# Kernel optimization log

Measured on AMD Instinct MI355X. Metric: run time of the kernel, lower is better.

Reference implementation:

```python
import jax, jax.numpy as jnp
import numpy as np

N_EXPERTS = 8
TOP_K = 2

def setup_inputs() -> dict:
    key = jax.random.key(0)
    ks = jax.random.split(key, 7)
    d, h, e = 1024, 4096, N_EXPERTS
    x = jax.random.normal(ks[0], (4, 2048, d), dtype=jnp.float32)
    gate_w = jax.random.normal(ks[1], (d, e), dtype=jnp.float32) * (1.0 / np.sqrt(d))
    gate_b = jnp.zeros((e,), dtype=jnp.float32)
    w1 = jax.random.normal(ks[2], (e, d, h), dtype=jnp.float32) * (1.0 / np.sqrt(d))
    b1 = jnp.zeros((e, h), dtype=jnp.float32)
    w2 = jax.random.normal(ks[3], (e, h, d), dtype=jnp.float32) * (1.0 / np.sqrt(h))
    b2 = jnp.zeros((e, d), dtype=jnp.float32)
    return {"x": x, "gate_w": gate_w, "gate_b": gate_b,
            "w1": w1, "b1": b1, "w2": w2, "b2": b2}

def reference(x, gate_w, gate_b, w1, b1, w2, b2):
    B, T, C = x.shape
    xf = x.reshape(-1, C)                                  # [N, C]
    gate_logits = xf @ gate_w + gate_b                     # [N, E]
    top_vals, top_idx = jax.lax.top_k(gate_logits, TOP_K)  # [N, K]
    top_w = jax.nn.softmax(top_vals, axis=-1)              # softmax over selected logits
    out = jnp.zeros_like(xf)
    for i in range(N_EXPERTS):
        # per-token combine weight for expert i (0 if not in top-k)
        wi = jnp.sum(jnp.where(top_idx == i, top_w, 0.0), axis=-1)  # [N]
        h = jax.nn.gelu(xf @ w1[i] + b1[i], approximate=False)      # [N, 4C]
        y = h @ w2[i] + b2[i]                                       # [N, C]
        out = out + wi[:, None] * y
    return out.reshape(B, T, C)
```

## Files before the change

kernel.cpp:

```cpp
#include <hip/hip_runtime.h>
#include <math.h>


#define NTOK 8192
#define CDIM 1024
#define HDIM 4096
#define NEXP 8
#define MAXT2 71
#define MAXROWS2 (MAXT2 * 256)
#define G1BLK (MAXT2 * 16)
#define TRBLK 512

typedef unsigned short u16;
typedef __attribute__((ext_vector_type(8))) _Float16 half8;
typedef __attribute__((ext_vector_type(4))) float f32x4;

__device__ __forceinline__ u16 f2h(float f) {
    union { _Float16 h; u16 u; } cv; cv.h = (_Float16)f; return cv.u;
}
__device__ __forceinline__ float h2f(u16 u) {
    union { u16 u; _Float16 h; } cv; cv.u = u; return (float)cv.h;
}
__device__ __forceinline__ void gll16(const u16* g, u16* l) {
    __builtin_amdgcn_global_load_lds((__attribute__((address_space(1))) void*)(g),
                                     (__attribute__((address_space(3))) void*)(l),
                                     16, 0, 0);
}
__device__ __forceinline__ float gelu_f(float v) {
    float u = 0.70710678118654752f * v;
    float au = fabsf(u);
    float t = __builtin_amdgcn_rcpf(1.0f + 0.3275911f * au);
    float p = t * (0.254829592f + t * (-0.284496736f + t * (1.421413741f +
              t * (-1.453152027f + t * 1.061405429f))));
    float ea = __expf(-au * au);
    float er = 1.0f - p * ea;
    er = (u < 0.f) ? -er : er;
    return 0.5f * v * (1.0f + er);
}
__device__ __forceinline__ int xcd_remap(int lid, int nact) {
    int q = nact >> 3, r = nact & 7;
    int xcd = lid & 7, pos = lid >> 3;
    return (xcd < r) ? (xcd * (q + 1) + pos) : (r * (q + 1) + (xcd - r) * q + pos);
}
__device__ __forceinline__ int sched_nt(const int* __restrict__ cnt8) {
    int at = 0;
#pragma unroll
    for (int q = 0; q < NEXP; ++q) at += (cnt8[q] + 255) >> 8;
    return at;
}
__device__ __forceinline__ void sched_tile(const int* __restrict__ cnt8, int t,
                                           int& e, int& rt, int& prow, int& cnte) {
    int at = 0, ar = 0; e = -1; rt = 0; prow = 0; cnte = 0;
#pragma unroll
    for (int q = 0; q < NEXP; ++q) {
        int c = cnt8[q]; int ti = (c + 255) >> 8;
        if (e < 0 && t < at + ti) { e = q; rt = t - at; prow = ar; cnte = c; }
        at += ti; ar += ti * 256;
    }
}

__device__ __forceinline__ void route_body(
    int blk, const float* __restrict__ x, const float* __restrict__ gw,
    const float* __restrict__ gb, u16* __restrict__ xh,
    float2* __restrict__ rtw, int* __restrict__ choice)
{
    int tid = threadIdx.x, lane = tid & 63, wid = tid >> 6;
    int tok = blk * 4 + wid;
    const float* xr = x + (size_t)tok * CDIM;
    float a[NEXP];
#pragma unroll
    for (int e = 0; e < NEXP; e++) a[e] = 0.f;
#pragma unroll
    for (int j = 0; j < 4; j++) {
        int k0 = j * 256 + lane * 4;
        float4 xv = *reinterpret_cast<const float4*>(xr + k0);
        ushort4 hv;
        hv.x = f2h(xv.x); hv.y = f2h(xv.y); hv.z = f2h(xv.z); hv.w = f2h(xv.w);
        *reinterpret_cast<ushort4*>(xh + (size_t)tok * CDIM + k0) = hv;
        const float* gr = gw + (size_t)k0 * NEXP;
#pragma unroll
        for (int t = 0; t < 4; t++) {
            float xs = (t == 0) ? xv.x : (t == 1) ? xv.y : (t == 2) ? xv.z : xv.w;
            float4 g0 = *reinterpret_cast<const float4*>(gr + t * 8);
            float4 g1 = *reinterpret_cast<const float4*>(gr + t * 8 + 4);
            a[0] += xs * g0.x; a[1] += xs * g0.y; a[2] += xs * g0.z; a[3] += xs * g0.w;
            a[4] += xs * g1.x; a[5] += xs * g1.y; a[6] += xs * g1.z; a[7] += xs * g1.w;
        }
    }
#pragma unroll
    for (int ofs = 32; ofs >= 1; ofs >>= 1) {
#pragma unroll
        for (int e = 0; e < NEXP; e++) a[e] += __shfl_xor(a[e], ofs, 64);
    }
    if (lane == 0) {
#pragma unroll
        for (int e = 0; e < NEXP; e++) a[e] += gb[e];
        int i0 = 0; float v0 = a[0];
#pragma unroll
        for (int e = 1; e < NEXP; e++) if (a[e] > v0) { v0 = a[e]; i0 = e; }
        int i1 = -1; float v1 = -3.4e38f;
#pragma unroll
        for (int e = 0; e < NEXP; e++) if (e != i0 && a[e] > v1) { v1 = a[e]; i1 = e; }
        float t = expf(v1 - v0);
        float w0 = 1.f / (1.f + t);
        rtw[tok] = make_float2(w0, t * w0);
        choice[tok] = i0 | (i1 << 4);
    }
}

__device__ __forceinline__ void transpose_body4t(
    int bx, int by, int e, const float* __restrict__ src, u16* __restrict__ dst,
    int R, int S, u16* tile, int tid)
{
    const float* se = src + (size_t)e * R * S;
    u16* de = dst + (size_t)e * R * S;
    int c0 = bx * 256, r0 = by * 64;
    int bc = tid & 15, br = tid >> 4;
    int wr = tid & 15, cr = tid >> 4;
#pragma unroll
    for (int q = 0; q < 4; ++q) {
        int cq = c0 + q * 64;
        u16 h[4][4];
#pragma unroll
        for (int i = 0; i < 4; i++) {
            float4 v = *reinterpret_cast<const float4*>(
                se + (size_t)(r0 + 4 * br + i) * S + cq + 4 * bc);
            h[i][0] = f2h(v.x); h[i][1] = f2h(v.y); h[i][2] = f2h(v.z); h[i][3] = f2h(v.w);
        }
        if (q) __syncthreads();
#pragma unroll
        for (int j = 0; j < 4; j++) {
            ushort4 w;
            w.x = h[0][j]; w.y = h[1][j]; w.z = h[2][j]; w.w = h[3][j];
            int row = 4 * bc + j;
            *reinterpret_cast<ushort4*>(&tile[row * 64 + ((br ^ (row & 15)) << 2)]) = w;
        }
        __syncthreads();
#pragma unroll
        for (int i = 0; i < 4; i++) {
            int row = cr + 16 * i;
            ushort4 o = *reinterpret_cast<const ushort4*>(
                &tile[row * 64 + ((wr ^ (row & 15)) << 2)]);
            *reinterpret_cast<ushort4*>(de + (size_t)(cq + row) * R + r0 + 4 * wr) = o;
        }
    }
}

__global__ __launch_bounds__(256) void k_prep(
    const float* __restrict__ x, const float* __restrict__ gw,
    const float* __restrict__ gb, u16* __restrict__ xh,
    float2* __restrict__ rtw, int* __restrict__ choice,
    const float* __restrict__ w1, u16* __restrict__ w1t)
{
    __shared__ __align__(16) u16 tile[64 * 64];
    int z = blockIdx.z;
    int bxf = blockIdx.x;
    if (z == 0) {
        route_body(bxf, x, gw, gb, xh, rtw, choice);
    } else {
        int e = bxf >> 8, r = bxf & 255;
        transpose_body4t(r & 15, r >> 4, e, w1, w1t, CDIM, HDIM, tile, threadIdx.x);
    }
}

__global__ __launch_bounds__(256) void k_lists(
    const int* __restrict__ choice, int* __restrict__ cnt, int* __restrict__ lists)
{
    __shared__ int wsum[4];
    __shared__ int base;
    int e = blockIdx.x;
    int tid = threadIdx.x, lane = tid & 63, wv = tid >> 6;
    if (tid == 0) base = 0;
    __syncthreads();
    for (int t0 = 0; t0 < NTOK; t0 += 256) {
        int tok = t0 + tid;
        int ch = choice[tok];
        int i0 = ch & 15, i1 = (ch >> 4) & 15;
        int pred = (i0 == e || i1 == e) ? 1 : 0;
        int entry = tok * 2 + ((i0 == e) ? 0 : 1);
        unsigned long long m = __ballot(pred);
        int wpre = __popcll(m & ((1ull << lane) - 1ull));
        if (lane == 0) wsum[wv] = __popcll(m);
        __syncthreads();
        int pre = wpre;
#pragma unroll
        for (int w2 = 0; w2 < 4; ++w2) if (w2 < wv) pre += wsum[w2];
        int tot = wsum[0] + wsum[1] + wsum[2] + wsum[3];
        if (pred) lists[e * NTOK + base + pre] = entry;
        __syncthreads();
        if (tid == 0) base += tot;
        __syncthreads();
    }
    if (tid == 0) cnt[e] = base;
}

#define DSA(BUF, QR) do { \
    _Pragma("unroll") for (int fm_ = 0; fm_ < 4; ++fm_) { \
        af[fm_][0] = HA[aIdx0 + ((QR) * 4 + fm_) * 128 + (BUF) * 2048]; \
        af[fm_][1] = HA[aIdx1 + ((QR) * 4 + fm_) * 128 + (BUF) * 2048]; \
    } } while (0)

#define DSB(BUF, QC) do { \
    _Pragma("unroll") for (int fn_ = 0; fn_ < 2; ++fn_) { \
        bf[QC][fn_][0] = HB[bIdx0 + ((QC) * 2 + fn_) * 128 + (BUF) * 2048]; \
        bf[QC][fn_][1] = HB[bIdx1 + ((QC) * 2 + fn_) * 128 + (BUF) * 2048]; \
    } } while (0)

#define FFN_MFMA(QR, QC) do { \
    __builtin_amdgcn_s_setprio(1); \
    _Pragma("unroll") for (int fm_ = 0; fm_ < 4; ++fm_) \
    _Pragma("unroll") for (int fn_ = 0; fn_ < 2; ++fn_) { \
        acc[(QR) * 4 + fm_][(QC) * 2 + fn_] = __builtin_amdgcn_mfma_f32_16x16x32_f16( \
            bf[QC][fn_][0], af[fm_][0], acc[(QR) * 4 + fm_][(QC) * 2 + fn_], 0, 0, 0); \
        acc[(QR) * 4 + fm_][(QC) * 2 + fn_] = __builtin_amdgcn_mfma_f32_16x16x32_f16( \
            bf[QC][fn_][1], af[fm_][1], acc[(QR) * 4 + fm_][(QC) * 2 + fn_], 0, 0, 0); \
    } \
    __builtin_amdgcn_s_setprio(0); } while (0)

#define PUB()  __builtin_amdgcn_s_barrier()
#define PUBG() do { __builtin_amdgcn_s_barrier(); \
                    __builtin_amdgcn_sched_barrier(0); } while (0)
#define VMW4() asm volatile("s_waitcnt vmcnt(4)" ::: "memory")

#define STA(BUF, H) do { \
    gll16(pa[H][0], ldsA + (BUF) * 16384 + ((H) * 128 + wv * 16) * 64); pa[H][0] += 64; \
    gll16(pa[H][1], ldsA + (BUF) * 16384 + ((H) * 128 + wv * 16 + 8) * 64); pa[H][1] += 64; } while (0)

#define STB(BUF, H) do { \
    gll16(pb[H][0], ldsB + (BUF) * 16384 + ((H) * 128 + wv * 16) * 64); pb[H][0] += 64; \
    gll16(pb[H][1], ldsB + (BUF) * 16384 + ((H) * 128 + wv * 16 + 8) * 64); pb[H][1] += 64; } while (0)

#define FFN_KLOOP(NK) do { \
    STB(0, 0); STB(0, 1); STA(0, 0); STA(0, 1); STB(1, 0); STB(1, 1); \
    VMW4(); PUBG(); \
    for (int i_ = 0; i_ < (NK) / 2; ++i_) { \
        DSA(0, 0); DSB(0, 0); STA(1, 0);  PUB(); FFN_MFMA(0, 0); PUB(); \
        DSB(0, 1); STA(1, 1);             PUB(); FFN_MFMA(0, 1); PUBG(); \
        DSA(0, 1); STB(0, 0);             PUB(); FFN_MFMA(1, 0); PUB(); \
        STB(0, 1); VMW4();                PUB(); FFN_MFMA(1, 1); PUBG(); \
        DSA(1, 0); DSB(1, 0); STA(0, 0);  PUB(); FFN_MFMA(0, 0); PUB(); \
        DSB(1, 1); STA(0, 1);             PUB(); FFN_MFMA(0, 1); PUBG(); \
        DSA(1, 1); STB(1, 0);             PUB(); FFN_MFMA(1, 0); PUB(); \
        STB(1, 1); VMW4();                PUB(); FFN_MFMA(1, 1); PUBG(); \
    } } while (0)

__global__ __launch_bounds__(512, 2) void k_ffn1(
    const u16* __restrict__ xh, const u16* __restrict__ w1t,
    const float* __restrict__ b1, u16* __restrict__ hbuf,
    const int* __restrict__ ctrl, const int* __restrict__ lists,
    const float* __restrict__ w2, u16* __restrict__ w2t)
{
    extern __shared__ __align__(16) u16 lds[];
    int lid = blockIdx.x;
    int tid = threadIdx.x;
    if (lid >= G1BLK) {
        int tlid = lid - G1BLK;
        int e = tlid >> 6, by = tlid & 63;
        int half = tid >> 8, t2 = tid & 255;
        u16* mytile = lds + half * 4096;
#pragma unroll
        for (int c4 = 0; c4 < 2; ++c4)
            transpose_body4t(half * 2 + c4, by, e, w2, w2t, HDIM, CDIM, mytile, t2);
        return;
    }
    u16* ldsA = lds;
    u16* ldsB = lds + 2 * 256 * 64;
    const half8* HA = reinterpret_cast<const half8*>(ldsA);
    const half8* HB = reinterpret_cast<const half8*>(ldsB);
    const int* cnt8 = ctrl + 8;
    int nt = sched_nt(cnt8);
    int nact = nt * 16;
    if (lid >= nact) return;
    int w = xcd_remap(lid, nact);
    int nt8 = nt * 8;
    int byh = w / nt8;
    int rem = w - byh * nt8;
    int t = rem >> 3;
    int by = byh * 8 + (rem & 7);
    int e, rt, prow, cnte;
    sched_tile(cnt8, t, e, rt, prow, cnte);
    int n0 = by * 256;
    int lane = tid & 63, wv = tid >> 6;
    int wm = wv >> 2, wn = wv & 3;
    int lr = lane >> 3;
    int chunk = (lane & 7) ^ lr;
    const int* lrow = lists + e * NTOK + rt * 256;
    int first_ent = lists[e * NTOK];
    const u16* pa[2][2]; const u16* pb[2][2];
#pragma unroll
    for (int h = 0; h < 2; ++h)
#pragma unroll
        for (int g = 0; g < 2; ++g) {
            int r = h * 128 + wv * 16 + g * 8 + lr;
            int ent = (rt * 256 + r < cnte) ? lrow[r] : first_ent;
            int tok = ent >> 1;
            pa[h][g] = xh + (size_t)tok * CDIM + chunk * 8;
            pb[h][g] = w1t + (size_t)e * HDIM * CDIM + (size_t)(n0 + r) * CDIM + chunk * 8;
        }
    int aIdx0 = wm * 1024 + (lane & 15) * 8 + ((lane >> 4) ^ (lane & 7));
    int aIdx1 = wm * 1024 + (lane & 15) * 8 + (((lane >> 4) + 4) ^ (lane & 7));
    int bIdx0 = wn * 512 + (lane & 15) * 8 + ((lane >> 4) ^ (lane & 7));
    int bIdx1 = wn * 512 + (lane & 15) * 8 + (((lane >> 4) + 4) ^ (lane & 7));
    f32x4 acc[8][4];
#pragma unroll
    for (int m = 0; m < 8; ++m)
#pragma unroll
        for (int n = 0; n < 4; ++n) acc[m][n] = f32x4{0.f, 0.f, 0.f, 0.f};
    half8 af[4][2], bf[2][2][2];

    FFN_KLOOP(16);

    const f32x4* b1v = reinterpret_cast<const f32x4*>(b1 + (size_t)e * HDIM);
    f32x4 bv[4];
#pragma unroll
    for (int n = 0; n < 4; ++n)
        bv[n] = b1v[(n0 + wn * 64 + n * 16) / 4 + (lane >> 4)];
#pragma unroll
    for (int m = 0; m < 8; ++m) {
        int grow = prow + rt * 256 + wm * 128 + m * 16 + (lane & 15);
        u16* hr = hbuf + (size_t)grow * HDIM + n0 + wn * 64 + (lane >> 4) * 4;
#pragma unroll
        for (int n = 0; n < 4; ++n) {
            ushort4 o;
#pragma unroll
            for (int j = 0; j < 4; ++j)
                ((u16*)&o)[j] = f2h(gelu_f(acc[m][n][j] + bv[n][j]));
            *reinterpret_cast<ushort4*>(hr + n * 16) = o;
        }
    }
}

__global__ __launch_bounds__(512, 2) void k_ffn2(
    const u16* __restrict__ hbuf, const u16* __restrict__ w2t,
    const float* __restrict__ b2, u16* __restrict__ ybuf,
    const int* __restrict__ ctrl, const int* __restrict__ lists,
    const float2* __restrict__ rtw)
{
    extern __shared__ __align__(16) u16 lds[];
    u16* ldsA = lds;
    u16* ldsB = lds + 2 * 256 * 64;
    const half8* HA = reinterpret_cast<const half8*>(ldsA);
    const half8* HB = reinterpret_cast<const half8*>(ldsB);
    const int* cnt8 = ctrl + 8;
    int lid = ((int)blockIdx.z * gridDim.y + blockIdx.y) * gridDim.x + blockIdx.x;
    int nt = sched_nt(cnt8);
    int nact = nt * 16;
    if (lid >= nact) return;
    int w = xcd_remap(lid, nact);
    int nt4 = nt * 4;
    int kh = w / nt4;
    int rem = w - kh * nt4;
    int t = rem >> 2;
    int by = rem & 3;
    int e, rt, prow, cnte;
    sched_tile(cnt8, t, e, rt, prow, cnte);
    int n0 = by * 256;
    int tid = threadIdx.x, lane = tid & 63, wv = tid >> 6;
    int wm = wv >> 2, wn = wv & 3;
    int lr = lane >> 3;
    int chunk = (lane & 7) ^ lr;
    int rowbase = prow + rt * 256;
    const u16* pa[2][2]; const u16* pb[2][2];
#pragma unroll
    for (int h = 0; h < 2; ++h)
#pragma unroll
        for (int g = 0; g < 2; ++g) {
            int r = h * 128 + wv * 16 + g * 8 + lr;
            pa[h][g] = hbuf + (size_t)(rowbase + r) * HDIM + kh * 1024 + chunk * 8;
            pb[h][g] = w2t + (size_t)e * CDIM * HDIM + (size_t)(n0 + r) * HDIM + kh * 1024 + chunk * 8;
        }
    int aIdx0 = wm * 1024 + (lane & 15) * 8 + ((lane >> 4) ^ (lane & 7));
    int aIdx1 = wm * 1024 + (lane & 15) * 8 + (((lane >> 4) + 4) ^ (lane & 7));
    int bIdx0 = wn * 512 + (lane & 15) * 8 + ((lane >> 4) ^ (lane & 7));
    int bIdx1 = wn * 512 + (lane & 15) * 8 + (((lane >> 4) + 4) ^ (lane & 7));
    f32x4 acc[8][4];
#pragma unroll
    for (int m = 0; m < 8; ++m)
#pragma unroll
        for (int n = 0; n < 4; ++n) acc[m][n] = f32x4{0.f, 0.f, 0.f, 0.f};
    half8 af[4][2], bf[2][2][2];

    FFN_KLOOP(16);

    const f32x4* b2v = reinterpret_cast<const f32x4*>(b2 + (size_t)e * CDIM);
    f32x4 bv[4];
#pragma unroll
    for (int n = 0; n < 4; ++n)
        bv[n] = b2v[(n0 + wn * 64 + n * 16) / 4 + (lane >> 4)];
    const int* lrow = lists + e * NTOK;
#pragma unroll
    for (int m = 0; m < 8; ++m) {
        int p = rt * 256 + wm * 128 + m * 16 + (lane & 15);
        bool valid = p < cnte;
        int entry = valid ? lrow[p] : 0;
        float2 wpair = rtw[entry >> 1];
        float wgt = (entry & 1) ? wpair.y : wpair.x;
        u16* yb = ybuf + ((size_t)((entry & 1) * 4 + kh) * NTOK + (size_t)(entry >> 1)) * CDIM
                + n0 + wn * 64 + (lane >> 4) * 4;
#pragma unroll
        for (int n = 0; n < 4; ++n) {
            f32x4 v = acc[m][n];
            if (kh == 0) v = v + bv[n];
            v = v * wgt;
            ushort4 o;
#pragma unroll
            for (int j = 0; j < 4; ++j) ((u16*)&o)[j] = f2h(v[j]);
            if (valid) *reinterpret_cast<ushort4*>(yb + n * 16) = o;
        }
    }
}

__global__ __launch_bounds__(256) void k_combine(
    const u16* __restrict__ ybuf, float* __restrict__ out)
{
    size_t i = ((size_t)blockIdx.x * 256 + threadIdx.x) * 4;
    const size_t S = (size_t)NTOK * CDIM;
    float s0 = 0.f, s1 = 0.f, s2 = 0.f, s3 = 0.f;
#pragma unroll
    for (int sl = 0; sl < 8; ++sl) {
        ushort4 h = *reinterpret_cast<const ushort4*>(ybuf + sl * S + i);
        s0 += h2f(h.x); s1 += h2f(h.y); s2 += h2f(h.z); s3 += h2f(h.w);
    }
    f32x4 o; o[0] = s0; o[1] = s1; o[2] = s2; o[3] = s3;
    *reinterpret_cast<f32x4*>(out + i) = o;
}

extern "C" void kernel_launch(void* const* d_in, const int* in_sizes, int n_in,
                              void* d_out, int out_size, void* d_ws, size_t ws_size,
                              hipStream_t stream)
{
    const float* x  = (const float*)d_in[0];
    const float* gw = (const float*)d_in[1];
    const float* gb = (const float*)d_in[2];
    const float* w1 = (const float*)d_in[3];
    const float* b1 = (const float*)d_in[4];
    const float* w2 = (const float*)d_in[5];
    const float* b2 = (const float*)d_in[6];
    float* out = (float*)d_out;
    char* ws = (char*)d_ws;

    size_t off = 0;
    int*    ctrl  = (int*)(ws + off);    off += 4096;
    float2* rtw   = (float2*)(ws + off); off += (size_t)NTOK * 8;
    int*    choice= (int*)(ws + off);    off += (size_t)NTOK * 4;
    int*    lists = (int*)(ws + off);    off += (size_t)NEXP * NTOK * 4;
    u16*    xh    = (u16*)(ws + off);    off += (size_t)NTOK * CDIM * 2;
    u16*    w1t   = (u16*)(ws + off);    off += (size_t)NEXP * CDIM * HDIM * 2;
    u16*    w2t   = (u16*)(ws + off);    off += (size_t)NEXP * CDIM * HDIM * 2;
    u16*    hbuf  = (u16*)(ws + off);    off += (size_t)MAXROWS2 * HDIM * 2;
    u16*    ybuf  = (u16*)(ws + off);    off += (size_t)8 * NTOK * CDIM * 2;
    (void)ws_size; (void)in_sizes; (void)n_in; (void)out_size;

    hipFuncSetAttribute((const void*)k_ffn1, hipFuncAttributeMaxDynamicSharedMemorySize, 131072);
    hipFuncSetAttribute((const void*)k_ffn2, hipFuncAttributeMaxDynamicSharedMemorySize, 131072);

    k_prep<<<dim3(2048, 1, 2), 256, 0, stream>>>(x, gw, gb, xh, rtw, choice, w1, w1t);
    k_lists<<<dim3(NEXP), 256, 0, stream>>>(choice, ctrl + 8, lists);
    k_ffn1<<<dim3(G1BLK + TRBLK), 512, 131072, stream>>>(xh, w1t, b1, hbuf, ctrl, lists,
                                                         w2, w2t);
    k_ffn2<<<dim3(MAXT2, CDIM / 256, 4), 512, 131072, stream>>>(hbuf, w2t, b2, ybuf, ctrl, lists, rtw);
    k_combine<<<dim3(NTOK * CDIM / 1024), 256, 0, stream>>>(ybuf, out);
}
```

Baseline: 521.6 us.

## Rebalance FFN2 split-K with mixed heavy and light work units

Changes FFN2 from a fixed four-way K split to units that cover half of K (heavy blocks) and, when the number of units exceeds 512, splits the excess units into two quarter-K blocks. The intent is fewer blocks with longer K loops, which cuts partial-sum traffic and per-block overhead, while still keeping enough blocks to fill the GPU. Heavy blocks write zeros into the unused partial slice so the combine kernel stays unchanged. The cost is extra zero stores, plus a grid capped at 624 blocks that relies on the expected tile count.

```diff
diff --git a/kernel.cpp b/kernel.cpp
--- a/kernel.cpp
+++ b/kernel.cpp
@@ -10,6 +10,7 @@
 #define MAXROWS2 (MAXT2 * 256)
 #define G1BLK (MAXT2 * 16)
 #define TRBLK 512
+#define G2BLK 624
 
 typedef unsigned short u16;
 typedef __attribute__((ext_vector_type(8))) _Float16 half8;
@@ -342,19 +343,26 @@
     const half8* HA = reinterpret_cast<const half8*>(ldsA);
     const half8* HB = reinterpret_cast<const half8*>(ldsB);
     const int* cnt8 = ctrl + 8;
-    int lid = ((int)blockIdx.z * gridDim.y + blockIdx.y) * gridDim.x + blockIdx.x;
+    int lid = blockIdx.x;
     int nt = sched_nt(cnt8);
-    int nact = nt * 16;
+    int U = nt * 8;
+    int S = (U > 512) ? (U - 512) : 0;
+    int Hh = U - S;
+    int nact = Hh + 2 * S;
     if (lid >= nact) return;
-    int w = xcd_remap(lid, nact);
+    bool heavy = lid < Hh;
+    int u, qh;
+    if (heavy) { u = xcd_remap(lid, Hh); qh = 0; }
+    else { int l = lid - Hh; u = Hh + (l >> 1); qh = l & 1; }
     int nt4 = nt * 4;
-    int kh = w / nt4;
-    int rem = w - kh * nt4;
+    int kh = u / nt4;
+    int rem = u - kh * nt4;
     int t = rem >> 2;
     int by = rem & 3;
     int e, rt, prow, cnte;
     sched_tile(cnt8, t, e, rt, prow, cnte);
     int n0 = by * 256;
+    int koff = kh * 2048 + qh * 1024;
     int tid = threadIdx.x, lane = tid & 63, wv = tid >> 6;
     int wm = wv >> 2, wn = wv & 3;
     int lr = lane >> 3;
@@ -366,8 +374,8 @@
 #pragma unroll
         for (int g = 0; g < 2; ++g) {
             int r = h * 128 + wv * 16 + g * 8 + lr;
-            pa[h][g] = hbuf + (size_t)(rowbase + r) * HDIM + kh * 1024 + chunk * 8;
-            pb[h][g] = w2t + (size_t)e * CDIM * HDIM + (size_t)(n0 + r) * HDIM + kh * 1024 + chunk * 8;
+            pa[h][g] = hbuf + (size_t)(rowbase + r) * HDIM + koff + chunk * 8;
+            pb[h][g] = w2t + (size_t)e * CDIM * HDIM + (size_t)(n0 + r) * HDIM + koff + chunk * 8;
         }
     int aIdx0 = wm * 1024 + (lane & 15) * 8 + ((lane >> 4) ^ (lane & 7));
     int aIdx1 = wm * 1024 + (lane & 15) * 8 + (((lane >> 4) + 4) ^ (lane & 7));
@@ -380,7 +388,7 @@
         for (int n = 0; n < 4; ++n) acc[m][n] = f32x4{0.f, 0.f, 0.f, 0.f};
     half8 af[4][2], bf[2][2][2];
 
-    FFN_KLOOP(16);
+    if (heavy) { FFN_KLOOP(32); } else { FFN_KLOOP(16); }
 
     const f32x4* b2v = reinterpret_cast<const f32x4*>(b2 + (size_t)e * CDIM);
     f32x4 bv[4];
@@ -388,6 +396,8 @@
     for (int n = 0; n < 4; ++n)
         bv[n] = b2v[(n0 + wn * 64 + n * 16) / 4 + (lane >> 4)];
     const int* lrow = lists + e * NTOK;
+    const size_t SL = (size_t)NTOK * CDIM;
+    int q = 2 * kh + qh;
 #pragma unroll
     for (int m = 0; m < 8; ++m) {
         int p = rt * 256 + wm * 128 + m * 16 + (lane & 15);
@@ -395,17 +405,24 @@
         int entry = valid ? lrow[p] : 0;
         float2 wpair = rtw[entry >> 1];
         float wgt = (entry & 1) ? wpair.y : wpair.x;
-        u16* yb = ybuf + ((size_t)((entry & 1) * 4 + kh) * NTOK + (size_t)(entry >> 1)) * CDIM
-                + n0 + wn * 64 + (lane >> 4) * 4;
+        size_t base = (size_t)(entry >> 1) * CDIM + n0 + wn * 64 + (lane >> 4) * 4;
+        u16* yb = ybuf + ((size_t)((entry & 1) * 4 + q)) * SL + base;
+        u16* yz = ybuf + ((size_t)((entry & 1) * 4 + 2 * kh + 1)) * SL + base;
 #pragma unroll
         for (int n = 0; n < 4; ++n) {
             f32x4 v = acc[m][n];
-            if (kh == 0) v = v + bv[n];
+            if (koff == 0) v = v + bv[n];
             v = v * wgt;
             ushort4 o;
 #pragma unroll
             for (int j = 0; j < 4; ++j) ((u16*)&o)[j] = f2h(v[j]);
-            if (valid) *reinterpret_cast<ushort4*>(yb + n * 16) = o;
+            if (valid) {
+                *reinterpret_cast<ushort4*>(yb + n * 16) = o;
+                if (heavy) {
+                    ushort4 z; z.x = 0; z.y = 0; z.z = 0; z.w = 0;
+                    *reinterpret_cast<ushort4*>(yz + n * 16) = z;
+                }
+            }
         }
     }
 }
@@ -458,6 +475,6 @@
     k_lists<<<dim3(NEXP), 256, 0, stream>>>(choice, ctrl + 8, lists);
     k_ffn1<<<dim3(G1BLK + TRBLK), 512, 131072, stream>>>(xh, w1t, b1, hbuf, ctrl, lists,
                                                          w2, w2t);
-    k_ffn2<<<dim3(MAXT2, CDIM / 256, 4), 512, 131072, stream>>>(hbuf, w2t, b2, ybuf, ctrl, lists, rtw);
+    k_ffn2<<<dim3(G2BLK), 512, 131072, stream>>>(hbuf, w2t, b2, ybuf, ctrl, lists, rtw);
     k_combine<<<dim3(NTOK * CDIM / 1024), 256, 0, stream>>>(ybuf, out);
 }
```

After: 504.2 us (median of 2 runs). -3.3%, faster.
